# Kernel optimization log

Hardware: AMD Instinct MI355X
Metric: run time of the kernel (lower is better)

Reference implementation:

```python
import jax, jax.numpy as jnp
import numpy as np

B, N, D, H, K, MSL = 16, 512, 512, 8, 16, 512
HD = D // H
EPS = 1e-5


def _ln(x, g, b):
    m = jnp.mean(x, axis=-1, keepdims=True)
    v = jnp.mean((x - m) ** 2, axis=-1, keepdims=True)
    return (x - m) * jax.lax.rsqrt(v + EPS) * g + b


def setup_inputs() -> dict:
    key = jax.random.key(0)
    ks = jax.random.split(key, 12)
    s = 0.02
    d = {
        'x': jax.random.normal(ks[0], (B, N, D), jnp.float32),
        'wq': jax.random.normal(ks[1], (D, D), jnp.float32) * s,
        'bq': jnp.zeros((D,), jnp.float32),
        'wk': jax.random.normal(ks[2], (D, D), jnp.float32) * s,
        'bk': jnp.zeros((D,), jnp.float32),
        'wv': jax.random.normal(ks[3], (D, D), jnp.float32) * s,
        'bv': jnp.zeros((D,), jnp.float32),
        'wo': jax.random.normal(ks[4], (D, D), jnp.float32) * s,
        'bo': jnp.zeros((D,), jnp.float32),
        'g1': jnp.ones((D,), jnp.float32),
        'be1': jnp.zeros((D,), jnp.float32),
        'g2': jnp.ones((D,), jnp.float32),
        'be2': jnp.zeros((D,), jnp.float32),
        'w1': jax.random.normal(ks[5], (D, 4 * D), jnp.float32) * s,
        'bf1': jnp.zeros((4 * D,), jnp.float32),
        'w2': jax.random.normal(ks[6], (4 * D, D), jnp.float32) * s,
        'bf2': jnp.zeros((D,), jnp.float32),
        'rel_emb': jax.random.normal(ks[7], (2 * MSL - 1, H), jnp.float32) * s,
    }
    return d


def reference(x, wq, bq, wk, bk, wv, bv, wo, bo, g1, be1, g2, be2, w1, bf1, w2, bf2, rel_emb):
    # Pre-norm attention (dropout = identity, eval mode)
    xn = _ln(x, g1, be1)
    Q = (xn @ wq + bq).reshape(B, N, H, HD)
    Kh = (xn @ wk + bk).reshape(B, N, H, HD)
    V = (xn @ wv + bv).reshape(B, N, H, HD)
    scale = HD ** -0.5
    logits = jnp.einsum('bnhd,bmhd->bhnm', Q, Kh) * scale  # (B,H,N,N)
    # relative temporal bias
    pos = jnp.arange(N)
    drel = pos[None, :] - pos[:, None] + (MSL - 1)  # (N,N)
    bias = rel_emb[drel]  # (N,N,H)
    logits = logits + jnp.transpose(bias, (2, 0, 1))[None]
    # top-k sparsification + softmax over surviving entries only
    vals, idx = jax.lax.top_k(logits, K)  # (B,H,N,K)
    attn_k = jax.nn.softmax(vals, axis=-1)  # softmax over -inf-masked row == softmax over top-k
    # scatter probabilities back into dense (B,H,N,N) rows
    rows = jnp.zeros((B * H * N, N), logits.dtype)
    attn = jax.vmap(lambda r, i, v: r.at[i].set(v))(
        rows, idx.reshape(-1, K), attn_k.reshape(-1, K)
    ).reshape(B, H, N, N)
    out = jnp.einsum('bhnm,bmhd->bnhd', attn, V).reshape(B, N, D)
    out = out @ wo + bo
    x = x + out
    # feed-forward (GELU exact, matching torch default)
    xn2 = _ln(x, g2, be2)
    ff = jax.nn.gelu(xn2 @ w1 + bf1, approximate=False) @ w2 + bf2
    return x + ff
```

## Files before the change

### kernel.cpp

```cpp
#include <hip/hip_runtime.h>
#include <hip/hip_bf16.h>

#define BB 16
#define NN 512
#define DD 512
#define HH 8
#define HD 64
#define MM (BB*NN)
#define DFF 2048

typedef __attribute__((ext_vector_type(8))) short bf16x8;
typedef __attribute__((ext_vector_type(4))) float fx4;

static __device__ __forceinline__ unsigned short f2bf(float f) {
  unsigned u = __float_as_uint(f);
  u += 0x7FFFu + ((u >> 16) & 1u);
  return (unsigned short)(u >> 16);
}
static __device__ __forceinline__ float bf2f(unsigned short s) {
  return __uint_as_float(((unsigned)s) << 16);
}

static __device__ __forceinline__ void load_lds16(const unsigned short* g, unsigned short* l) {
  __builtin_amdgcn_global_load_lds(
      (const __attribute__((address_space(1))) void*)g,
      (__attribute__((address_space(3))) void*)l, 16, 0, 0);
}

__global__ void transpose_bf16(const float* __restrict__ in, unsigned short* __restrict__ out,
                               int K, int N) {
  __shared__ float tl[32][33];
  int tx = threadIdx.x, ty = threadIdx.y;
  int x0 = blockIdx.x * 32, y0 = blockIdx.y * 32;
  #pragma unroll
  for (int i = 0; i < 4; i++)
    tl[ty + i*8][tx] = in[(size_t)(y0 + ty + i*8) * N + x0 + tx];
  __syncthreads();
  #pragma unroll
  for (int i = 0; i < 4; i++)
    out[(size_t)(x0 + ty + i*8) * K + y0 + tx] = f2bf(tl[tx][ty + i*8]);
}

__global__ void concat_bias(const float* __restrict__ bq, const float* __restrict__ bk,
                            const float* __restrict__ bv, float* __restrict__ o) {
  int t = blockIdx.x * 256 + threadIdx.x;
  if (t < 512) o[t] = bq[t];
  else if (t < 1024) o[t] = bk[t - 512];
  else if (t < 1536) o[t] = bv[t - 1024];
}

__global__ __launch_bounds__(256) void ln_kernel(const float* __restrict__ X,
                                                 const float* __restrict__ g,
                                                 const float* __restrict__ be,
                                                 unsigned short* __restrict__ O) {
  int w = threadIdx.x >> 6, l = threadIdx.x & 63;
  size_t row = (size_t)blockIdx.x * 4 + w;
  const float* xr = X + row * 512;
  fx4 a = *(const fx4*)(xr + l*4);
  fx4 c = *(const fx4*)(xr + 256 + l*4);
  float s = a[0]+a[1]+a[2]+a[3] + c[0]+c[1]+c[2]+c[3];
  float q = a[0]*a[0]+a[1]*a[1]+a[2]*a[2]+a[3]*a[3]
          + c[0]*c[0]+c[1]*c[1]+c[2]*c[2]+c[3]*c[3];
  #pragma unroll
  for (int s2 = 1; s2 < 64; s2 <<= 1) { s += __shfl_xor(s, s2); q += __shfl_xor(q, s2); }
  float mean = s * (1.0f/512.0f);
  float var  = q * (1.0f/512.0f) - mean*mean;
  float rs = rsqrtf(var + 1e-5f);
  fx4 ga = *(const fx4*)(g + l*4);
  fx4 gc = *(const fx4*)(g + 256 + l*4);
  fx4 ba = *(const fx4*)(be + l*4);
  fx4 bc = *(const fx4*)(be + 256 + l*4);
  ushort4 o1, o2;
  o1.x = f2bf((a[0]-mean)*rs*ga[0] + ba[0]);
  o1.y = f2bf((a[1]-mean)*rs*ga[1] + ba[1]);
  o1.z = f2bf((a[2]-mean)*rs*ga[2] + ba[2]);
  o1.w = f2bf((a[3]-mean)*rs*ga[3] + ba[3]);
  o2.x = f2bf((c[0]-mean)*rs*gc[0] + bc[0]);
  o2.y = f2bf((c[1]-mean)*rs*gc[1] + bc[1]);
  o2.z = f2bf((c[2]-mean)*rs*gc[2] + bc[2]);
  o2.w = f2bf((c[3]-mean)*rs*gc[3] + bc[3]);
  *(ushort4*)(O + row*512 + l*4) = o1;
  *(ushort4*)(O + row*512 + 256 + l*4) = o2;
}

template<int MODE, int TN>
__global__ __launch_bounds__(256) void gemm_kernel(
    const unsigned short* __restrict__ A,
    const unsigned short* __restrict__ Bm,
    const float* __restrict__ bias,
    const float* resid,
    void* C,
    int M, int N, int K) {
  constexpr int MI = (TN == 128) ? 4 : 2;
  constexpr int WM = (TN == 128) ? 64 : 32;
  __shared__ unsigned short As[128*32];
  __shared__ unsigned short Bs[TN*32];
  int m0 = blockIdx.y * 128, n0 = blockIdx.x * TN;
  int t = threadIdx.x;
  int w = t >> 6, l = t & 63;
  int wm = (TN == 128) ? (w >> 1) : w;
  int wn = (TN == 128) ? (w & 1) : 0;
  int lid = l & 15, quad = l >> 4;
  int lrow = l >> 2, lch = l & 3;

  const unsigned short* gA0 = A  + (size_t)(m0 + w*16 + lrow)*K + lch*8;
  const unsigned short* gA1 = gA0 + (size_t)64*K;
  const unsigned short* gB0 = Bm + (size_t)(n0 + w*16 + lrow)*K + lch*8;
  const unsigned short* gB1 = (TN == 128) ? gB0 + (size_t)64*K : nullptr;
  unsigned short* lA0 = As + w*512;
  unsigned short* lA1 = As + 2048 + w*512;
  unsigned short* lB0 = Bs + w*512;
  unsigned short* lB1 = (TN == 128) ? Bs + 2048 + w*512 : nullptr;

  fx4 acc[MI][4];
  #pragma unroll
  for (int i = 0; i < MI; i++)
    #pragma unroll
    for (int j = 0; j < 4; j++) acc[i][j] = (fx4){0.f,0.f,0.f,0.f};

  for (int k0 = 0; k0 < K; k0 += 32) {
    load_lds16(gA0, lA0);
    load_lds16(gA1, lA1);
    load_lds16(gB0, lB0);
    if constexpr (TN == 128) load_lds16(gB1, lB1);
    gA0 += 32; gA1 += 32; gB0 += 32;
    if constexpr (TN == 128) gB1 += 32;
    __syncthreads();
    bf16x8 af[MI], bf[4];
    #pragma unroll
    for (int i = 0; i < MI; i++)
      af[i] = *(const bf16x8*)(As + (wm*WM + i*16 + lid)*32 + quad*8);
    #pragma unroll
    for (int j = 0; j < 4; j++)
      bf[j] = *(const bf16x8*)(Bs + (wn*64 + j*16 + lid)*32 + quad*8);
    #pragma unroll
    for (int i = 0; i < MI; i++)
      #pragma unroll
      for (int j = 0; j < 4; j++)
        acc[i][j] = __builtin_amdgcn_mfma_f32_16x16x32_bf16(af[i], bf[j], acc[i][j], 0, 0, 0);
    __syncthreads();
  }

  #pragma unroll
  for (int i = 0; i < MI; i++) {
    #pragma unroll
    for (int j = 0; j < 4; j++) {
      int col = n0 + wn*64 + j*16 + lid;
      float bv = bias[col];
      #pragma unroll
      for (int r = 0; r < 4; r++) {
        int row = m0 + wm*WM + i*16 + quad*4 + r;
        float v = acc[i][j][r] + bv;
        if (MODE == 0) {
          if (col < 512) v *= 0.125f;
          ((unsigned short*)C)[(size_t)row*N + col] = f2bf(v);
        } else if (MODE == 1 || MODE == 3) {
          v += resid[(size_t)row*N + col];
          ((float*)C)[(size_t)row*N + col] = v;
        } else {
          float gl = 0.5f * v * (1.0f + erff(v * 0.70710678118654752f));
          ((unsigned short*)C)[(size_t)row*N + col] = f2bf(gl);
        }
      }
    }
  }
}

__global__ __launch_bounds__(256) void attn_kernel(
    const unsigned short* __restrict__ QKV,
    const float* __restrict__ rel_emb,
    unsigned short* __restrict__ Aout) {
  __shared__ float smem[10752];
  unsigned short* Ks = (unsigned short*)smem;
  float* bias_s = smem + 9216;
  float* pr = smem + 10240;
  int blk = blockIdx.x;
  int q0 = (blk & 7) << 6;
  int bh = blk >> 3;
  int b = bh >> 3, h = bh & 7;
  int t = threadIdx.x;
  int w = t >> 6, l = t & 63;
  int lid = l & 15, quad = l >> 4;

  for (int i = t; i < 1023; i += 256) bias_s[i] = rel_emb[i*8 + h];

  int qn = q0 + w*16 + lid;
  const unsigned short* qp = QKV + ((size_t)(b*512 + qn))*1536 + h*64 + quad*8;
  bf16x8 qf0 = *(const bf16x8*)qp;
  bf16x8 qf1 = *(const bf16x8*)(qp + 32);

  fx4 acc[32];
  #pragma unroll
  for (int i = 0; i < 32; i++) acc[i] = (fx4){0.f,0.f,0.f,0.f};

  #pragma unroll
  for (int half = 0; half < 2; half++) {
    __syncthreads();
    #pragma unroll
    for (int i = 0; i < 8; i++) {
      int c = t + i*256;
      int row = c >> 3, ch = c & 7;
      uint4 d = *(const uint4*)(QKV + ((size_t)(b*512 + half*256 + row))*1536 + 512 + h*64 + ch*8);
      *(uint4*)(Ks + row*72 + ch*8) = d;
    }
    __syncthreads();
    #pragma unroll
    for (int kt = 0; kt < 16; kt++) {
      const unsigned short* kp = Ks + (kt*16 + lid)*72 + quad*8;
      bf16x8 kb0 = *(const bf16x8*)kp;
      bf16x8 kb1 = *(const bf16x8*)(kp + 32);
      int ai = half*16 + kt;
      acc[ai] = __builtin_amdgcn_mfma_f32_16x16x32_bf16(qf0, kb0, acc[ai], 0, 0, 0);
      acc[ai] = __builtin_amdgcn_mfma_f32_16x16x32_bf16(qf1, kb1, acc[ai], 0, 0, 0);
    }
  }

  int nb = q0 + w*16 + quad*4;
  #pragma unroll
  for (int kt = 0; kt < 32; kt++) {
    int m = kt*16 + lid;
    int bidx = m - nb + 511;
    #pragma unroll
    for (int r = 0; r < 4; r++) {
      float v = acc[kt][r] + bias_s[bidx - r];
      unsigned mu = __float_as_uint(v);
      mu = (mu & 0x80000000u) ? ~mu : (mu | 0x80000000u);
      acc[kt][r] = __uint_as_float((mu & 0xFFFFFE00u) | (unsigned)(511 - m));
    }
  }

  unsigned lo0=0, lo1=0, lo2=0, lo3=0;
  unsigned hi0=0xFFFFFFFFu, hi1=0xFFFFFFFFu, hi2=0xFFFFFFFFu, hi3=0xFFFFFFFFu;
  unsigned th0=0, th1=0, th2=0, th3=0;
  unsigned done = 0;
  #pragma unroll 1
  for (int it = 0; it < 34; ++it) {
    unsigned d_;
    d_ = hi0-lo0; unsigned mid0 = lo0 + (d_>>1) + (d_&1u);
    d_ = hi1-lo1; unsigned mid1 = lo1 + (d_>>1) + (d_&1u);
    d_ = hi2-lo2; unsigned mid2 = lo2 + (d_>>1) + (d_&1u);
    d_ = hi3-lo3; unsigned mid3 = lo3 + (d_>>1) + (d_&1u);
    unsigned c0=0, c1=0, c2=0, c3=0;
    #pragma unroll
    for (int kt = 0; kt < 32; kt++) {
      c0 += (__float_as_uint(acc[kt][0]) >= mid0);
      c1 += (__float_as_uint(acc[kt][1]) >= mid1);
      c2 += (__float_as_uint(acc[kt][2]) >= mid2);
      c3 += (__float_as_uint(acc[kt][3]) >= mid3);
    }
    unsigned p01 = c0 | (c1 << 16);
    unsigned p23 = c2 | (c3 << 16);
    #pragma unroll
    for (int s2 = 1; s2 < 16; s2 <<= 1) {
      p01 += __shfl_xor(p01, s2);
      p23 += __shfl_xor(p23, s2);
    }
    unsigned C0 = p01 & 0xFFFFu, C1 = p01 >> 16;
    unsigned C2 = p23 & 0xFFFFu, C3 = p23 >> 16;
    { bool f = !(done & 1u); bool e = f && (C0 == 16u);
      th0 = e ? mid0 : th0; done |= e ? 1u : 0u;
      lo0 = (f && C0 > 16u) ? mid0 : lo0; hi0 = (f && C0 < 16u) ? mid0 : hi0; }
    { bool f = !(done & 2u); bool e = f && (C1 == 16u);
      th1 = e ? mid1 : th1; done |= e ? 2u : 0u;
      lo1 = (f && C1 > 16u) ? mid1 : lo1; hi1 = (f && C1 < 16u) ? mid1 : hi1; }
    { bool f = !(done & 4u); bool e = f && (C2 == 16u);
      th2 = e ? mid2 : th2; done |= e ? 4u : 0u;
      lo2 = (f && C2 > 16u) ? mid2 : lo2; hi2 = (f && C2 < 16u) ? mid2 : hi2; }
    { bool f = !(done & 8u); bool e = f && (C3 == 16u);
      th3 = e ? mid3 : th3; done |= e ? 8u : 0u;
      lo3 = (f && C3 > 16u) ? mid3 : lo3; hi3 = (f && C3 < 16u) ? mid3 : hi3; }
    if (__all((int)(done == 15u))) break;
  }

  float* prE = pr + w*128 + quad*32;
  int*   prM = (int*)prE + 16;
  unsigned below = (1u << lid) - 1u;
  #pragma unroll
  for (int r = 0; r < 4; r++) {
    unsigned thr = (r==0) ? th0 : (r==1) ? th1 : (r==2) ? th2 : th3;
    int base = 0;
    #pragma unroll
    for (int kt = 0; kt < 32; kt++) {
      unsigned u = __float_as_uint(acc[kt][r]);
      bool sel = u >= thr;
      unsigned long long bm = __ballot(sel);
      unsigned gm = (unsigned)(bm >> (quad*16)) & 0xFFFFu;
      if (sel) {
        int slot = base + __popc(gm & below);
        unsigned vu = u & 0xFFFFFE00u;
        vu = (vu & 0x80000000u) ? (vu & 0x7FFFFFFFu) : ~vu;
        float e = exp2f(__uint_as_float(vu) * 1.44269504f);
        if (slot < 16) { prE[slot] = e; prM[slot] = 511 - (int)(u & 0x1FFu); }
      }
      base += __popc(gm);
    }
    __threadfence_block();
    int n = nb + r;
    float o0=0.f, o1=0.f, o2=0.f, o3=0.f, es=0.f;
    #pragma unroll
    for (int k2 = 0; k2 < 16; k2++) {
      float e = prE[k2];
      int m = prM[k2];
      const unsigned short* vp = QKV + ((size_t)(b*512 + m))*1536 + 1024 + h*64 + lid*4;
      ushort4 v4 = *(const ushort4*)vp;
      es += e;
      o0 += e * bf2f(v4.x); o1 += e * bf2f(v4.y);
      o2 += e * bf2f(v4.z); o3 += e * bf2f(v4.w);
    }
    float inv = 1.0f / es;
    ushort4 ov;
    ov.x = f2bf(o0*inv); ov.y = f2bf(o1*inv);
    ov.z = f2bf(o2*inv); ov.w = f2bf(o3*inv);
    *(ushort4*)(Aout + ((size_t)(b*512 + n))*512 + h*64 + lid*4) = ov;
    __threadfence_block();
  }
}

extern "C" void kernel_launch(void* const* d_in, const int* in_sizes, int n_in,
                              void* d_out, int out_size, void* d_ws, size_t ws_size,
                              hipStream_t stream) {
  const float* x   = (const float*)d_in[0];
  const float* wq  = (const float*)d_in[1];
  const float* bq  = (const float*)d_in[2];
  const float* wk  = (const float*)d_in[3];
  const float* bk  = (const float*)d_in[4];
  const float* wv  = (const float*)d_in[5];
  const float* bv  = (const float*)d_in[6];
  const float* wo  = (const float*)d_in[7];
  const float* bo  = (const float*)d_in[8];
  const float* g1  = (const float*)d_in[9];
  const float* be1 = (const float*)d_in[10];
  const float* g2  = (const float*)d_in[11];
  const float* be2 = (const float*)d_in[12];
  const float* w1  = (const float*)d_in[13];
  const float* bf1 = (const float*)d_in[14];
  const float* w2  = (const float*)d_in[15];
  const float* bf2 = (const float*)d_in[16];
  const float* rel = (const float*)d_in[17];

  char* p = (char*)d_ws;
  size_t off = 0;
  auto alloc = [&](size_t bytes) {
    size_t cur = off;
    off += (bytes + 255) & ~(size_t)255;
    return (void*)(p + cur);
  };
  unsigned short* wqkvT = (unsigned short*)alloc((size_t)1536*512*2);
  unsigned short* woT   = (unsigned short*)alloc((size_t)512*512*2);
  unsigned short* w1T   = (unsigned short*)alloc((size_t)2048*512*2);
  unsigned short* w2T   = (unsigned short*)alloc((size_t)512*2048*2);
  float*          bqkv  = (float*)alloc(1536*4);
  unsigned short* R1    = (unsigned short*)alloc((size_t)MM*512*2);
  unsigned short* R2    = (unsigned short*)alloc((size_t)MM*2048*2);

  unsigned short* xn1  = R1;
  unsigned short* aout = R1;
  unsigned short* xn2  = R1;
  unsigned short* qkvb = R2;
  unsigned short* hbuf = R2;
  float*          x2   = (float*)d_out;
  (void)ws_size; (void)in_sizes; (void)n_in; (void)out_size;

  dim3 tb(32, 8);
  transpose_bf16<<<dim3(16, 16), tb, 0, stream>>>(wq, wqkvT,             512, 512);
  transpose_bf16<<<dim3(16, 16), tb, 0, stream>>>(wk, wqkvT + 512*512,   512, 512);
  transpose_bf16<<<dim3(16, 16), tb, 0, stream>>>(wv, wqkvT + 2*512*512, 512, 512);
  transpose_bf16<<<dim3(16, 16), tb, 0, stream>>>(wo, woT,               512, 512);
  transpose_bf16<<<dim3(64, 16), tb, 0, stream>>>(w1, w1T,  512, 2048);
  transpose_bf16<<<dim3(16, 64), tb, 0, stream>>>(w2, w2T, 2048,  512);
  concat_bias<<<6, 256, 0, stream>>>(bq, bk, bv, bqkv);

  ln_kernel<<<2048, 256, 0, stream>>>(x, g1, be1, xn1);
  gemm_kernel<0,128><<<dim3(12, 64), 256, 0, stream>>>(xn1, wqkvT, bqkv, nullptr, qkvb, MM, 1536, 512);
  attn_kernel<<<1024, 256, 0, stream>>>(qkvb, rel, aout);
  gemm_kernel<1,64><<<dim3(8, 64), 256, 0, stream>>>(aout, woT, bo, x, x2, MM, 512, 512);
  ln_kernel<<<2048, 256, 0, stream>>>(x2, g2, be2, xn2);
  gemm_kernel<2,128><<<dim3(16, 64), 256, 0, stream>>>(xn2, w1T, bf1, nullptr, hbuf, MM, 2048, 512);
  gemm_kernel<3,64><<<dim3(8, 64), 256, 0, stream>>>(hbuf, w2T, bf2, x2, (float*)d_out, MM, 512, 2048);
}
```

Measured before the change: 427.4 us.

## Retile GEMMs to 64-row blocks with K=64 swizzled LDS and fuse transposes

The GEMM kernel now uses 64-row M tiles with a 64-wide K step per iteration, halving the number of barrier pairs per K loop. LDS columns are XOR-swizzled by row to avoid bank conflicts on the fragment reads, and the grid doubles in the M direction to raise occupancy on the many CUs. Separately, six weight-transpose launches are merged into one kernel to cut launch overhead. The smaller M tile lowers per-block reuse of B data and adds global traffic in exchange for more parallelism.

```diff
diff --git a/kernel.cpp b/kernel.cpp
--- a/kernel.cpp
+++ b/kernel.cpp
@@ -27,18 +27,35 @@
       (__attribute__((address_space(3))) void*)l, 16, 0, 0);
 }
 
-__global__ void transpose_bf16(const float* __restrict__ in, unsigned short* __restrict__ out,
-                               int K, int N) {
+__global__ void transpose_all(const float* __restrict__ wq, const float* __restrict__ wk,
+                              const float* __restrict__ wv, const float* __restrict__ wo,
+                              const float* __restrict__ w1, const float* __restrict__ w2,
+                              unsigned short* __restrict__ wqkvT, unsigned short* __restrict__ woT,
+                              unsigned short* __restrict__ w1T, unsigned short* __restrict__ w2T) {
   __shared__ float tl[32][33];
+  int id = blockIdx.x;
+  const float* src; unsigned short* dst; int K, N, bx, by;
+  if (id < 1024) {
+    int m = id >> 8, tt = id & 255;
+    src = (m == 0) ? wq : (m == 1) ? wk : (m == 2) ? wv : wo;
+    dst = (m == 3) ? woT : wqkvT + m * 512 * 512;
+    K = 512; N = 512; bx = tt & 15; by = tt >> 4;
+  } else if (id < 2048) {
+    int tt = id - 1024;
+    src = w1; dst = w1T; K = 512; N = 2048; bx = tt & 63; by = tt >> 6;
+  } else {
+    int tt = id - 2048;
+    src = w2; dst = w2T; K = 2048; N = 512; bx = tt & 15; by = tt >> 4;
+  }
   int tx = threadIdx.x, ty = threadIdx.y;
-  int x0 = blockIdx.x * 32, y0 = blockIdx.y * 32;
+  int x0 = bx * 32, y0 = by * 32;
   #pragma unroll
   for (int i = 0; i < 4; i++)
-    tl[ty + i*8][tx] = in[(size_t)(y0 + ty + i*8) * N + x0 + tx];
+    tl[ty + i*8][tx] = src[(size_t)(y0 + ty + i*8) * N + x0 + tx];
   __syncthreads();
   #pragma unroll
   for (int i = 0; i < 4; i++)
-    out[(size_t)(x0 + ty + i*8) * K + y0 + tx] = f2bf(tl[tx][ty + i*8]);
+    dst[(size_t)(x0 + ty + i*8) * K + y0 + tx] = f2bf(tl[tx][ty + i*8]);
 }
 
 __global__ void concat_bias(const float* __restrict__ bq, const float* __restrict__ bk,
@@ -91,26 +108,26 @@
     const float* resid,
     void* C,
     int M, int N, int K) {
-  constexpr int MI = (TN == 128) ? 4 : 2;
-  constexpr int WM = (TN == 128) ? 64 : 32;
-  __shared__ unsigned short As[128*32];
-  __shared__ unsigned short Bs[TN*32];
-  int m0 = blockIdx.y * 128, n0 = blockIdx.x * TN;
+  constexpr int MI  = (TN == 128) ? 2 : 1;
+  constexpr int BW  = (TN == 128) ? 32 : 16;
+  constexpr int NBI = (TN == 128) ? 4 : 2;
+  __shared__ unsigned short As[64*64];
+  __shared__ unsigned short Bs[TN*64];
+  int m0 = blockIdx.y * 64, n0 = blockIdx.x * TN;
   int t = threadIdx.x;
   int w = t >> 6, l = t & 63;
   int wm = (TN == 128) ? (w >> 1) : w;
   int wn = (TN == 128) ? (w & 1) : 0;
   int lid = l & 15, quad = l >> 4;
-  int lrow = l >> 2, lch = l & 3;
-
-  const unsigned short* gA0 = A  + (size_t)(m0 + w*16 + lrow)*K + lch*8;
-  const unsigned short* gA1 = gA0 + (size_t)64*K;
-  const unsigned short* gB0 = Bm + (size_t)(n0 + w*16 + lrow)*K + lch*8;
-  const unsigned short* gB1 = (TN == 128) ? gB0 + (size_t)64*K : nullptr;
-  unsigned short* lA0 = As + w*512;
-  unsigned short* lA1 = As + 2048 + w*512;
-  unsigned short* lB0 = Bs + w*512;
-  unsigned short* lB1 = (TN == 128) ? Bs + 2048 + w*512 : nullptr;
+  int lrow = l >> 3, lch = (l & 7) ^ lrow;
+
+  const unsigned short* gA = A  + (size_t)(m0 + w*16 + lrow)*K + lch*8;
+  const unsigned short* gB = Bm + (size_t)(n0 + w*BW + lrow)*K + lch*8;
+  unsigned short* lA0 = As + (w*16    )*64;
+  unsigned short* lA1 = As + (w*16 + 8)*64;
+  unsigned short* lB[NBI];
+  #pragma unroll
+  for (int i = 0; i < NBI; i++) lB[i] = Bs + (w*BW + i*8)*64;
 
   fx4 acc[MI][4];
   #pragma unroll
@@ -118,26 +135,35 @@
     #pragma unroll
     for (int j = 0; j < 4; j++) acc[i][j] = (fx4){0.f,0.f,0.f,0.f};
 
-  for (int k0 = 0; k0 < K; k0 += 32) {
-    load_lds16(gA0, lA0);
-    load_lds16(gA1, lA1);
-    load_lds16(gB0, lB0);
-    if constexpr (TN == 128) load_lds16(gB1, lB1);
-    gA0 += 32; gA1 += 32; gB0 += 32;
-    if constexpr (TN == 128) gB1 += 32;
+  int xA = (lid & 7) * 8;
+
+  for (int k0 = 0; k0 < K; k0 += 64) {
+    load_lds16(gA,       lA0);
+    load_lds16(gA + 8*K, lA1);
+    #pragma unroll
+    for (int i = 0; i < NBI; i++) load_lds16(gB + (size_t)(i*8)*K, lB[i]);
+    gA += 64; gB += 64;
     __syncthreads();
-    bf16x8 af[MI], bf[4];
-    #pragma unroll
-    for (int i = 0; i < MI; i++)
-      af[i] = *(const bf16x8*)(As + (wm*WM + i*16 + lid)*32 + quad*8);
-    #pragma unroll
-    for (int j = 0; j < 4; j++)
-      bf[j] = *(const bf16x8*)(Bs + (wn*64 + j*16 + lid)*32 + quad*8);
-    #pragma unroll
-    for (int i = 0; i < MI; i++)
+    #pragma unroll
+    for (int s = 0; s < 2; s++) {
+      int cbase = (s*4 + quad) * 8;
+      bf16x8 af[MI], bf[4];
       #pragma unroll
-      for (int j = 0; j < 4; j++)
-        acc[i][j] = __builtin_amdgcn_mfma_f32_16x16x32_bf16(af[i], bf[j], acc[i][j], 0, 0, 0);
+      for (int i = 0; i < MI; i++) {
+        int ra = wm*(MI*16) + i*16 + lid;
+        af[i] = *(const bf16x8*)(As + ra*64 + (cbase ^ xA));
+      }
+      #pragma unroll
+      for (int j = 0; j < 4; j++) {
+        int rb = wn*64 + j*16 + lid;
+        bf[j] = *(const bf16x8*)(Bs + rb*64 + (cbase ^ xA));
+      }
+      #pragma unroll
+      for (int i = 0; i < MI; i++)
+        #pragma unroll
+        for (int j = 0; j < 4; j++)
+          acc[i][j] = __builtin_amdgcn_mfma_f32_16x16x32_bf16(af[i], bf[j], acc[i][j], 0, 0, 0);
+    }
     __syncthreads();
   }
 
@@ -149,7 +175,7 @@
       float bv = bias[col];
       #pragma unroll
       for (int r = 0; r < 4; r++) {
-        int row = m0 + wm*WM + i*16 + quad*4 + r;
+        int row = m0 + wm*(MI*16) + i*16 + quad*4 + r;
         float v = acc[i][j][r] + bv;
         if (MODE == 0) {
           if (col < 512) v *= 0.125f;
@@ -361,20 +387,15 @@
   float*          x2   = (float*)d_out;
   (void)ws_size; (void)in_sizes; (void)n_in; (void)out_size;
 
-  dim3 tb(32, 8);
-  transpose_bf16<<<dim3(16, 16), tb, 0, stream>>>(wq, wqkvT,             512, 512);
-  transpose_bf16<<<dim3(16, 16), tb, 0, stream>>>(wk, wqkvT + 512*512,   512, 512);
-  transpose_bf16<<<dim3(16, 16), tb, 0, stream>>>(wv, wqkvT + 2*512*512, 512, 512);
-  transpose_bf16<<<dim3(16, 16), tb, 0, stream>>>(wo, woT,               512, 512);
-  transpose_bf16<<<dim3(64, 16), tb, 0, stream>>>(w1, w1T,  512, 2048);
-  transpose_bf16<<<dim3(16, 64), tb, 0, stream>>>(w2, w2T, 2048,  512);
+  transpose_all<<<3072, dim3(32, 8), 0, stream>>>(wq, wk, wv, wo, w1, w2,
+                                                  wqkvT, woT, w1T, w2T);
   concat_bias<<<6, 256, 0, stream>>>(bq, bk, bv, bqkv);
 
   ln_kernel<<<2048, 256, 0, stream>>>(x, g1, be1, xn1);
-  gemm_kernel<0,128><<<dim3(12, 64), 256, 0, stream>>>(xn1, wqkvT, bqkv, nullptr, qkvb, MM, 1536, 512);
+  gemm_kernel<0,128><<<dim3(12, 128), 256, 0, stream>>>(xn1, wqkvT, bqkv, nullptr, qkvb, MM, 1536, 512);
   attn_kernel<<<1024, 256, 0, stream>>>(qkvb, rel, aout);
-  gemm_kernel<1,64><<<dim3(8, 64), 256, 0, stream>>>(aout, woT, bo, x, x2, MM, 512, 512);
+  gemm_kernel<1,64><<<dim3(8, 128), 256, 0, stream>>>(aout, woT, bo, x, x2, MM, 512, 512);
   ln_kernel<<<2048, 256, 0, stream>>>(x2, g2, be2, xn2);
-  gemm_kernel<2,128><<<dim3(16, 64), 256, 0, stream>>>(xn2, w1T, bf1, nullptr, hbuf, MM, 2048, 512);
-  gemm_kernel<3,64><<<dim3(8, 64), 256, 0, stream>>>(hbuf, w2T, bf2, x2, (float*)d_out, MM, 512, 2048);
-}
+  gemm_kernel<2,128><<<dim3(16, 128), 256, 0, stream>>>(xn2, w1T, bf1, nullptr, hbuf, MM, 2048, 512);
+  gemm_kernel<3,64><<<dim3(8, 128), 256, 0, stream>>>(hbuf, w2T, bf2, x2, (float*)d_out, MM, 512, 2048);
+}
```

After: 411.6 us. 1.04x faster.
